# Kernel optimization log

Hardware: AMD Instinct MI355X
Metric: run time of the kernel (lower is better)

## Reference

```python
import jax, jax.numpy as jnp
import numpy as np

B, N, C = 8, 4096, 1024
H = 16
D = C // H  # head_dim = 64
SCALE = D ** -0.5


def setup_inputs() -> dict:
    key = jax.random.key(0)
    ks = jax.random.split(key, 5)
    s = 0.02
    return {
        "x": jax.random.normal(ks[0], (B, N, C), dtype=jnp.float32),
        "Wq": jax.random.normal(ks[1], (C, C), dtype=jnp.float32) * s,
        "Wk": jax.random.normal(ks[2], (C, C), dtype=jnp.float32) * s,
        "Wv": jax.random.normal(ks[3], (C, C), dtype=jnp.float32) * s,
        "Wp": jax.random.normal(ks[4], (C, C), dtype=jnp.float32) * s,
        "bp": jnp.zeros((C,), dtype=jnp.float32),
    }


def reference(x, Wq, Wk, Wv, Wp, bp):
    b, n, c = x.shape
    # nn.Linear: y = x @ W^T (no bias for q/k/v)
    def split_heads(y):
        # (B,N,C) -> (B,N,H,D) -> permute(0,2,3,1) -> (B,H,D,N)
        return jnp.transpose(y.reshape(b, n, H, D), (0, 2, 3, 1))

    q = split_heads(x @ Wq.T)  # (B,H,D,N)
    k = split_heads(x @ Wk.T)  # (B,H,D,N)
    v = split_heads(x @ Wv.T)  # (B,H,D,N)

    # attn over head_dim (faithful to source layout): (B,H,D,D)
    attn = jnp.einsum('bhdn,bhen->bhde', q, k) * SCALE
    attn = jax.nn.softmax(attn, axis=-1)
    # (B,H,D,D) @ (B,H,D,N) -> (B,H,D,N); transpose(1,2) -> (B,D,H,N); reshape (B,N,C)
    out = jnp.einsum('bhde,bhen->bhdn', attn, v)
    out = jnp.transpose(out, (0, 2, 1, 3)).reshape(b, n, c)
    return out @ Wp.T + bp
```

## Files before the change

kernel.cpp:

```cpp
#include <hip/hip_runtime.h>


typedef __attribute__((ext_vector_type(4))) float f32x4;
typedef __attribute__((ext_vector_type(8))) _Float16 f16x8;
typedef __attribute__((ext_vector_type(4))) unsigned short u16x4;
typedef __attribute__((ext_vector_type(8))) unsigned short u16x8;

__device__ __forceinline__ unsigned short f2h(float f) {
  union { _Float16 h; unsigned short u; } v;
  v.h = (_Float16)f;
  return v.u;
}

__global__ void cvt_f32_f16(const float* __restrict__ in, unsigned short* __restrict__ out, int n) {
  int i = (blockIdx.x * blockDim.x + threadIdx.x) * 4;
  if (i >= n) return;
  float4 v = *(const float4*)(in + i);
  u16x4 o;
  o.x = f2h(v.x); o.y = f2h(v.y); o.z = f2h(v.z); o.w = f2h(v.w);
  *(u16x4*)(out + i) = o;
}

__global__ void cvt4_f32_f16(const float* __restrict__ s0, const float* __restrict__ s1,
                             const float* __restrict__ s2, const float* __restrict__ s3,
                             unsigned short* __restrict__ d0, unsigned short* __restrict__ d1,
                             unsigned short* __restrict__ d2, unsigned short* __restrict__ d3) {
  const float* src; unsigned short* dst;
  switch (blockIdx.y) {
    case 0: src = s0; dst = d0; break;
    case 1: src = s1; dst = d1; break;
    case 2: src = s2; dst = d2; break;
    default: src = s3; dst = d3; break;
  }
  int i = (blockIdx.x * blockDim.x + threadIdx.x) * 4;
  float4 v = *(const float4*)(src + i);
  u16x4 o;
  o.x = f2h(v.x); o.y = f2h(v.y); o.z = f2h(v.z); o.w = f2h(v.w);
  *(u16x4*)(dst + i) = o;
}

enum { EPI_QKV = 0, EPI_F32_BIAS = 2 };

#define GLD(SRC, DST)                                                                   \
  __builtin_amdgcn_global_load_lds((const __attribute__((address_space(1))) void*)(SRC), \
                                   (__attribute__((address_space(3))) void*)(DST), 16, 0, 0)
#define SBAR() asm volatile("s_barrier" ::: "memory")

template <int EPI>
__global__ __launch_bounds__(512, 2) void gemm256(const unsigned short* __restrict__ A,
                                                  const unsigned short* __restrict__ Bt,
                                                  void* __restrict__ Cv,
                                                  const float* __restrict__ bias,
                                                  const int M, const int N, const int K) {
  __shared__ unsigned short lds[EPI == EPI_QKV ? 73728 : 65536];
  const int tid = threadIdx.x;
  const int w = tid >> 6, lane = tid & 63;
  const int quad = lane >> 4, l15 = lane & 15;
  const int wm = w >> 2, wn = w & 3;

  const int nt_n = N >> 8;
  const int cpx = (int)gridDim.x >> 3;
  const int xcd = (int)blockIdx.x & 7;
  const int lx = (int)blockIdx.x >> 3;
  const int strip = cpx / nt_n;
  const int per_bng = strip * 4;
  const int bng = lx / per_bng;
  const int r1 = lx - bng * per_bng;
  const int bmg = r1 >> 5;
  const int r2 = r1 & 31;
  const int bm = xcd * strip + bmg * 8 + (r2 & 7);
  const int bn = bng * 4 + (r2 >> 3);
  const int m0 = bm << 8, n0 = bn << 8;

  const int srow = lane >> 3;
  const unsigned short* aSrc = A + (size_t)(m0 + srow) * K + (((lane & 7) ^ srow) << 3);
  const unsigned short* bSrc = Bt + (size_t)(n0 + srow) * K + (((lane & 7) ^ srow) << 3);

  const int rbA = (w >> 2) * 128 + (w & 3) * 16;
  const int rbB = (w >> 1) * 64 + (w & 1) * 16;

  const int arow = (wm * 128 + l15) << 6;
  const int brow = (wn * 64 + l15) << 6;
  const int ak0 = (quad ^ (l15 & 7)) << 3;
  const int ak1 = ((4 + quad) ^ (l15 & 7)) << 3;

  f32x4 acc[8][4];
#pragma unroll
  for (int i = 0; i < 8; ++i)
#pragma unroll
    for (int j = 0; j < 4; ++j) acc[i][j] = f32x4{0.f, 0.f, 0.f, 0.f};
  f16x8 af[4][2], bf[2][2][2];

  const int NT = K >> 6;

  GLD(aSrc + (size_t)rbA * K, &lds[rbA * 64]);
  GLD(aSrc + (size_t)(rbA + 8) * K, &lds[(rbA + 8) * 64]);
  GLD(bSrc + (size_t)rbB * K, &lds[16384 + rbB * 64]);
  GLD(bSrc + (size_t)(rbB + 8) * K, &lds[16384 + (rbB + 8) * 64]);
  GLD(bSrc + (size_t)(rbB + 32) * K, &lds[16384 + (rbB + 32) * 64]);
  GLD(bSrc + (size_t)(rbB + 40) * K, &lds[16384 + (rbB + 40) * 64]);
  GLD(aSrc + (size_t)(rbA + 64) * K, &lds[(rbA + 64) * 64]);
  GLD(aSrc + (size_t)(rbA + 72) * K, &lds[(rbA + 72) * 64]);
  asm volatile("s_waitcnt vmcnt(4)" ::: "memory");
  SBAR();

  for (int t = 0; t < NT; ++t) {
    const int db = (t & 1) << 15;
    const int sb = ((t + 1) & 1) << 15;
    const int ks = (t + 1) << 6;
    const bool st = (t + 1) < NT;

#pragma unroll
    for (int mi = 0; mi < 4; ++mi) {
      af[mi][0] = *(const f16x8*)&lds[db + arow + mi * 1024 + ak0];
      af[mi][1] = *(const f16x8*)&lds[db + arow + mi * 1024 + ak1];
    }
#pragma unroll
    for (int nn = 0; nn < 2; ++nn) {
      bf[0][nn][0] = *(const f16x8*)&lds[db + 16384 + brow + nn * 1024 + ak0];
      bf[0][nn][1] = *(const f16x8*)&lds[db + 16384 + brow + nn * 1024 + ak1];
    }
    if (st) {
      GLD(aSrc + (size_t)rbA * K + ks, &lds[sb + rbA * 64]);
      GLD(aSrc + (size_t)(rbA + 8) * K + ks, &lds[sb + (rbA + 8) * 64]);
      GLD(bSrc + (size_t)rbB * K + ks, &lds[sb + 16384 + rbB * 64]);
      GLD(bSrc + (size_t)(rbB + 8) * K + ks, &lds[sb + 16384 + (rbB + 8) * 64]);
      GLD(bSrc + (size_t)(rbB + 32) * K + ks, &lds[sb + 16384 + (rbB + 32) * 64]);
      GLD(bSrc + (size_t)(rbB + 40) * K + ks, &lds[sb + 16384 + (rbB + 40) * 64]);
      GLD(aSrc + (size_t)(rbA + 64) * K + ks, &lds[sb + (rbA + 64) * 64]);
      GLD(aSrc + (size_t)(rbA + 72) * K + ks, &lds[sb + (rbA + 72) * 64]);
    }
    SBAR();
    __builtin_amdgcn_s_setprio(1);
#pragma unroll
    for (int s = 0; s < 2; ++s)
#pragma unroll
      for (int mi = 0; mi < 4; ++mi)
#pragma unroll
        for (int nn = 0; nn < 2; ++nn)
          acc[mi][nn] = __builtin_amdgcn_mfma_f32_16x16x32_f16(af[mi][s], bf[0][nn][s], acc[mi][nn], 0, 0, 0);
    __builtin_amdgcn_s_setprio(0);
    if (st) asm volatile("s_waitcnt vmcnt(10)" ::: "memory");
    else    asm volatile("s_waitcnt vmcnt(2)" ::: "memory");
    SBAR();

#pragma unroll
    for (int nn = 0; nn < 2; ++nn) {
      bf[1][nn][0] = *(const f16x8*)&lds[db + 16384 + brow + 2048 + nn * 1024 + ak0];
      bf[1][nn][1] = *(const f16x8*)&lds[db + 16384 + brow + 2048 + nn * 1024 + ak1];
    }
    SBAR();
    __builtin_amdgcn_s_setprio(1);
#pragma unroll
    for (int s = 0; s < 2; ++s)
#pragma unroll
      for (int mi = 0; mi < 4; ++mi)
#pragma unroll
        for (int nn = 0; nn < 2; ++nn)
          acc[mi][2 + nn] = __builtin_amdgcn_mfma_f32_16x16x32_f16(af[mi][s], bf[1][nn][s], acc[mi][2 + nn], 0, 0, 0);
    __builtin_amdgcn_s_setprio(0);
    if (st) asm volatile("s_waitcnt vmcnt(8)" ::: "memory");
    else    asm volatile("s_waitcnt vmcnt(0)" ::: "memory");
    SBAR();

#pragma unroll
    for (int mi = 0; mi < 4; ++mi) {
      af[mi][0] = *(const f16x8*)&lds[db + arow + 4096 + mi * 1024 + ak0];
      af[mi][1] = *(const f16x8*)&lds[db + arow + 4096 + mi * 1024 + ak1];
    }
    SBAR();
    __builtin_amdgcn_s_setprio(1);
#pragma unroll
    for (int s = 0; s < 2; ++s)
#pragma unroll
      for (int mi = 0; mi < 4; ++mi)
#pragma unroll
        for (int nn = 0; nn < 2; ++nn)
          acc[4 + mi][nn] = __builtin_amdgcn_mfma_f32_16x16x32_f16(af[mi][s], bf[0][nn][s], acc[4 + mi][nn], 0, 0, 0);
#pragma unroll
    for (int s = 0; s < 2; ++s)
#pragma unroll
      for (int mi = 0; mi < 4; ++mi)
#pragma unroll
        for (int nn = 0; nn < 2; ++nn)
          acc[4 + mi][2 + nn] = __builtin_amdgcn_mfma_f32_16x16x32_f16(af[mi][s], bf[1][nn][s], acc[4 + mi][2 + nn], 0, 0, 0);
    __builtin_amdgcn_s_setprio(0);
    if (st) asm volatile("s_waitcnt vmcnt(4)" ::: "memory");
    SBAR();
  }

  if (EPI == EPI_F32_BIAS) {
    float* C = (float*)Cv;
#pragma unroll
    for (int ni = 0; ni < 4; ++ni) {
      const int col = n0 + wn * 64 + ni * 16 + l15;
      const float bv = bias[col];
#pragma unroll
      for (int mi = 0; mi < 8; ++mi)
#pragma unroll
        for (int rr = 0; rr < 4; ++rr) {
          const int row = m0 + wm * 128 + mi * 16 + quad * 4 + rr;
          C[(size_t)row * N + col] = acc[mi][ni][rr] + bv;
        }
    }
  } else {
    unsigned short* C = (unsigned short*)Cv;
    const bool isT = (n0 < 2048);
    unsigned short* wreg = &lds[w * 9216];
    if (isT) {
#pragma unroll
      for (int mi = 0; mi < 8; ++mi)
#pragma unroll
        for (int ni = 0; ni < 4; ++ni) {
          u16x4 pk;
          pk.x = f2h(acc[mi][ni][0]); pk.y = f2h(acc[mi][ni][1]);
          pk.z = f2h(acc[mi][ni][2]); pk.w = f2h(acc[mi][ni][3]);
          *(u16x4*)&wreg[(ni * 16 + l15) * 136 + mi * 16 + quad * 4] = pk;
        }
#pragma unroll
      for (int p = 0; p < 16; ++p) {
        const int ch = p * 4 + quad;
        u16x8 v = *(const u16x8*)&wreg[ch * 136 + l15 * 8];
        *(u16x8*)&C[(size_t)(n0 + wn * 64 + ch) * M + m0 + wm * 128 + l15 * 8] = v;
      }
    } else {
#pragma unroll
      for (int mi = 0; mi < 8; ++mi)
#pragma unroll
        for (int ni = 0; ni < 4; ++ni)
#pragma unroll
          for (int rr = 0; rr < 4; ++rr)
            wreg[(mi * 16 + quad * 4 + rr) * 72 + ni * 16 + l15] = f2h(acc[mi][ni][rr]);
#pragma unroll
      for (int p = 0; p < 16; ++p) {
        const int tok = p * 8 + (lane >> 3);
        u16x8 v = *(const u16x8*)&wreg[tok * 72 + (lane & 7) * 8];
        *(u16x8*)&C[(size_t)2048 * M + (size_t)(m0 + wm * 128 + tok) * 1024 +
                    (n0 - 2048) + wn * 64 + (lane & 7) * 8] = v;
      }
    }
  }
}

__global__ __launch_bounds__(256) void attn_logits(const unsigned short* __restrict__ qkt,
                                                   float* __restrict__ pbuf) {
  const int h = blockIdx.x, b = blockIdx.y, s = blockIdx.z;
  const int tid = threadIdx.x;
  const int wave = tid >> 6, lane = tid & 63;
  const int quad = lane >> 4, l15 = lane & 15;

  f32x4 acc[4];
#pragma unroll
  for (int t = 0; t < 4; t++) acc[t] = f32x4{0.f, 0.f, 0.f, 0.f};

  const unsigned short* qp =
      qkt + (size_t)(h * 64 + wave * 16 + l15) * 32768 + b * 4096 + s * 256 + quad * 8;
  const unsigned short* kp[4];
#pragma unroll
  for (int et = 0; et < 4; et++)
    kp[et] = qkt + (size_t)(1024 + h * 64 + et * 16 + l15) * 32768 + b * 4096 + s * 256 + quad * 8;

#pragma unroll 2
  for (int k0 = 0; k0 < 256; k0 += 32) {
    f16x8 aq = *(const f16x8*)(qp + k0);
#pragma unroll
    for (int et = 0; et < 4; et++) {
      f16x8 bk = *(const f16x8*)(kp[et] + k0);
      acc[et] = __builtin_amdgcn_mfma_f32_16x16x32_f16(aq, bk, acc[et], 0, 0, 0);
    }
  }

  float* pb = pbuf + ((size_t)(b * 16 + h) * 16 + s) * 4096;
#pragma unroll
  for (int et = 0; et < 4; et++)
#pragma unroll
    for (int rr = 0; rr < 4; rr++)
      pb[(wave * 16 + quad * 4 + rr) * 64 + et * 16 + l15] = acc[et][rr];
}

__global__ __launch_bounds__(256) void attn_softmax(const float* __restrict__ pbuf,
                                                    unsigned short* __restrict__ pP) {
  const int bh = blockIdx.x >> 2, dg = blockIdx.x & 3;
  const int t = threadIdx.x;
  const int d = dg * 16 + (t >> 4), e4 = t & 15;
  const float* pb = pbuf + (size_t)bh * 65536 + d * 64 + e4 * 4;

  float v[4] = {0.f, 0.f, 0.f, 0.f};
  for (int s = 0; s < 16; s++) {
    float4 tt = *(const float4*)(pb + s * 4096);
    v[0] += tt.x; v[1] += tt.y; v[2] += tt.z; v[3] += tt.w;
  }
#pragma unroll
  for (int i = 0; i < 4; i++) v[i] *= 0.125f;

  float m = fmaxf(fmaxf(v[0], v[1]), fmaxf(v[2], v[3]));
#pragma unroll
  for (int o = 1; o < 16; o <<= 1) m = fmaxf(m, __shfl_xor(m, o, 16));
  float sum = 0.f;
#pragma unroll
  for (int i = 0; i < 4; i++) {
    v[i] = __expf(v[i] - m);
    sum += v[i];
  }
#pragma unroll
  for (int o = 1; o < 16; o <<= 1) sum += __shfl_xor(sum, o, 16);
  const float inv = 1.f / sum;

  u16x4 o4;
  o4.x = f2h(v[0] * inv); o4.y = f2h(v[1] * inv);
  o4.z = f2h(v[2] * inv); o4.w = f2h(v[3] * inv);
  *(u16x4*)(pP + (size_t)bh * 4096 + d * 64 + e4 * 4) = o4;
}

__global__ __launch_bounds__(256) void attn_pv(const unsigned short* __restrict__ pP,
                                               const unsigned short* __restrict__ vbuf,
                                               unsigned short* __restrict__ y) {
  __shared__ unsigned short tile[64 * 264];
  const int h = blockIdx.x, b = blockIdx.y, s = blockIdx.z;
  const int tid = threadIdx.x;
  const int wave = tid >> 6, lane = tid & 63;
  const int quad = lane >> 4, l15 = lane & 15;
  const int bh = b * 16 + h;

  const unsigned short* pp = pP + (size_t)bh * 4096 + (wave * 16 + l15) * 64 + quad * 8;
  f16x8 pa0 = *(const f16x8*)(pp);
  f16x8 pa1 = *(const f16x8*)(pp + 32);

  const unsigned short* vb =
      vbuf + (size_t)(b * 4096 + s * 256 + l15) * 1024 + h * 64 + quad * 8;

#pragma unroll 4
  for (int nt = 0; nt < 16; nt++) {
    const unsigned short* vp = vb + (size_t)nt * 16 * 1024;
    f16x8 v0 = *(const f16x8*)(vp);
    f16x8 v1 = *(const f16x8*)(vp + 32);
    f32x4 o = f32x4{0.f, 0.f, 0.f, 0.f};
    o = __builtin_amdgcn_mfma_f32_16x16x32_f16(pa0, v0, o, 0, 0, 0);
    o = __builtin_amdgcn_mfma_f32_16x16x32_f16(pa1, v1, o, 0, 0, 0);
    const int ncol = nt * 16 + l15;
#pragma unroll
    for (int rr = 0; rr < 4; rr++)
      tile[(wave * 16 + quad * 4 + rr) * 264 + ncol] = f2h(o[rr]);
  }
  __syncthreads();

  const int d = tid & 63, cc = tid >> 6;
  const int R = d * 64 + h * 4 + (s >> 2);
  unsigned short* dst =
      y + (size_t)b * 4194304 + (size_t)R * 1024 + (s & 3) * 256 + cc * 64;
  const unsigned short* srcp = &tile[d * 264 + cc * 64];
#pragma unroll
  for (int i = 0; i < 8; i++)
    *(u16x8*)(dst + i * 8) = *(const u16x8*)(srcp + i * 8);
}

extern "C" void kernel_launch(void* const* d_in, const int* in_sizes, int n_in, void* d_out,
                              int out_size, void* d_ws, size_t ws_size, hipStream_t stream) {
  (void)in_sizes; (void)n_in; (void)out_size; (void)ws_size;
  const float* x = (const float*)d_in[0];
  const float* Wq = (const float*)d_in[1];
  const float* Wk = (const float*)d_in[2];
  const float* Wv = (const float*)d_in[3];
  const float* Wp = (const float*)d_in[4];
  const float* bp = (const float*)d_in[5];

  char* ws = (char*)d_ws;
  unsigned short* xb = (unsigned short*)(ws);
  float* pbuf = (float*)(ws);
  unsigned short* yb = xb;
  unsigned short* qkt = (unsigned short*)(ws + (size_t)67108864);
  unsigned short* pP = qkt;
  unsigned short* vbuf = (unsigned short*)(ws + (size_t)201326592);
  unsigned short* wqkv = (unsigned short*)(ws + (size_t)268435456);
  unsigned short* wp = (unsigned short*)(ws + (size_t)274726912);

  cvt_f32_f16<<<32768, 256, 0, stream>>>(x, xb, 33554432);
  cvt4_f32_f16<<<dim3(1024, 4), 256, 0, stream>>>(Wq, Wk, Wv, Wp, wqkv, wqkv + 1048576,
                                                  wqkv + 2097152, wp);

  gemm256<EPI_QKV><<<1536, 512, 0, stream>>>(xb, wqkv, qkt, nullptr, 32768, 3072, 1024);

  attn_logits<<<dim3(16, 8, 16), 256, 0, stream>>>(qkt, pbuf);
  attn_softmax<<<512, 256, 0, stream>>>(pbuf, pP);
  attn_pv<<<dim3(16, 8, 16), 256, 0, stream>>>(pP, vbuf, yb);

  gemm256<EPI_F32_BIAS><<<512, 512, 0, stream>>>(yb, wp, (float*)d_out, bp, 32768, 1024, 1024);
}
```

Measured before the change: 645.8 us.

## Restructure GEMM main loop to prefetch next tile fragments and cut barriers

Reorganizes the double-buffered GEMM K-loop to hold separate register fragments for the low and high A halves and the two B halves. The first fragments of the next tile are loaded from LDS before the last MFMA block of the current iteration. The per-iteration barriers drop from five to two, and the global loads are split around the first MFMA block. The aim is to remove LDS-read stalls and barrier overhead between MFMA groups. In exchange it uses more fragment registers, which may lower occupancy. It also waits for all global loads (vmcnt(0)) at the end of each iteration, which may expose memory latency.

```diff
diff --git a/kernel.cpp b/kernel.cpp
--- a/kernel.cpp
+++ b/kernel.cpp
@@ -89,7 +89,7 @@
   for (int i = 0; i < 8; ++i)
 #pragma unroll
     for (int j = 0; j < 4; ++j) acc[i][j] = f32x4{0.f, 0.f, 0.f, 0.f};
-  f16x8 af[4][2], bf[2][2][2];
+  f16x8 al[4][2], ah[4][2], b0[2][2], b1[2][2];
 
   const int NT = K >> 6;
 
@@ -101,8 +101,18 @@
   GLD(bSrc + (size_t)(rbB + 40) * K, &lds[16384 + (rbB + 40) * 64]);
   GLD(aSrc + (size_t)(rbA + 64) * K, &lds[(rbA + 64) * 64]);
   GLD(aSrc + (size_t)(rbA + 72) * K, &lds[(rbA + 72) * 64]);
-  asm volatile("s_waitcnt vmcnt(4)" ::: "memory");
+  asm volatile("s_waitcnt vmcnt(0)" ::: "memory");
   SBAR();
+#pragma unroll
+  for (int mi = 0; mi < 4; ++mi) {
+    al[mi][0] = *(const f16x8*)&lds[arow + mi * 1024 + ak0];
+    al[mi][1] = *(const f16x8*)&lds[arow + mi * 1024 + ak1];
+  }
+#pragma unroll
+  for (int nn = 0; nn < 2; ++nn) {
+    b0[nn][0] = *(const f16x8*)&lds[16384 + brow + nn * 1024 + ak0];
+    b0[nn][1] = *(const f16x8*)&lds[16384 + brow + nn * 1024 + ak1];
+  }
 
   for (int t = 0; t < NT; ++t) {
     const int db = (t & 1) << 15;
@@ -111,26 +121,38 @@
     const bool st = (t + 1) < NT;
 
 #pragma unroll
+    for (int nn = 0; nn < 2; ++nn) {
+      b1[nn][0] = *(const f16x8*)&lds[db + 16384 + brow + 2048 + nn * 1024 + ak0];
+      b1[nn][1] = *(const f16x8*)&lds[db + 16384 + brow + 2048 + nn * 1024 + ak1];
+    }
+#pragma unroll
     for (int mi = 0; mi < 4; ++mi) {
-      af[mi][0] = *(const f16x8*)&lds[db + arow + mi * 1024 + ak0];
-      af[mi][1] = *(const f16x8*)&lds[db + arow + mi * 1024 + ak1];
-    }
-#pragma unroll
-    for (int nn = 0; nn < 2; ++nn) {
-      bf[0][nn][0] = *(const f16x8*)&lds[db + 16384 + brow + nn * 1024 + ak0];
-      bf[0][nn][1] = *(const f16x8*)&lds[db + 16384 + brow + nn * 1024 + ak1];
+      ah[mi][0] = *(const f16x8*)&lds[db + arow + 4096 + mi * 1024 + ak0];
+      ah[mi][1] = *(const f16x8*)&lds[db + arow + 4096 + mi * 1024 + ak1];
     }
     if (st) {
       GLD(aSrc + (size_t)rbA * K + ks, &lds[sb + rbA * 64]);
       GLD(aSrc + (size_t)(rbA + 8) * K + ks, &lds[sb + (rbA + 8) * 64]);
       GLD(bSrc + (size_t)rbB * K + ks, &lds[sb + 16384 + rbB * 64]);
       GLD(bSrc + (size_t)(rbB + 8) * K + ks, &lds[sb + 16384 + (rbB + 8) * 64]);
+    }
+
+    __builtin_amdgcn_s_setprio(1);
+#pragma unroll
+    for (int s = 0; s < 2; ++s)
+#pragma unroll
+      for (int mi = 0; mi < 4; ++mi)
+#pragma unroll
+        for (int nn = 0; nn < 2; ++nn)
+          acc[mi][nn] = __builtin_amdgcn_mfma_f32_16x16x32_f16(al[mi][s], b0[nn][s], acc[mi][nn], 0, 0, 0);
+    __builtin_amdgcn_s_setprio(0);
+    if (st) {
       GLD(bSrc + (size_t)(rbB + 32) * K + ks, &lds[sb + 16384 + (rbB + 32) * 64]);
       GLD(bSrc + (size_t)(rbB + 40) * K + ks, &lds[sb + 16384 + (rbB + 40) * 64]);
       GLD(aSrc + (size_t)(rbA + 64) * K + ks, &lds[sb + (rbA + 64) * 64]);
       GLD(aSrc + (size_t)(rbA + 72) * K + ks, &lds[sb + (rbA + 72) * 64]);
     }
-    SBAR();
+
     __builtin_amdgcn_s_setprio(1);
 #pragma unroll
     for (int s = 0; s < 2; ++s)
@@ -138,18 +160,9 @@
       for (int mi = 0; mi < 4; ++mi)
 #pragma unroll
         for (int nn = 0; nn < 2; ++nn)
-          acc[mi][nn] = __builtin_amdgcn_mfma_f32_16x16x32_f16(af[mi][s], bf[0][nn][s], acc[mi][nn], 0, 0, 0);
+          acc[mi][2 + nn] = __builtin_amdgcn_mfma_f32_16x16x32_f16(al[mi][s], b1[nn][s], acc[mi][2 + nn], 0, 0, 0);
     __builtin_amdgcn_s_setprio(0);
-    if (st) asm volatile("s_waitcnt vmcnt(10)" ::: "memory");
-    else    asm volatile("s_waitcnt vmcnt(2)" ::: "memory");
-    SBAR();
-
-#pragma unroll
-    for (int nn = 0; nn < 2; ++nn) {
-      bf[1][nn][0] = *(const f16x8*)&lds[db + 16384 + brow + 2048 + nn * 1024 + ak0];
-      bf[1][nn][1] = *(const f16x8*)&lds[db + 16384 + brow + 2048 + nn * 1024 + ak1];
-    }
-    SBAR();
+
     __builtin_amdgcn_s_setprio(1);
 #pragma unroll
     for (int s = 0; s < 2; ++s)
@@ -157,18 +170,26 @@
       for (int mi = 0; mi < 4; ++mi)
 #pragma unroll
         for (int nn = 0; nn < 2; ++nn)
-          acc[mi][2 + nn] = __builtin_amdgcn_mfma_f32_16x16x32_f16(af[mi][s], bf[1][nn][s], acc[mi][2 + nn], 0, 0, 0);
+          acc[4 + mi][nn] = __builtin_amdgcn_mfma_f32_16x16x32_f16(ah[mi][s], b0[nn][s], acc[4 + mi][nn], 0, 0, 0);
     __builtin_amdgcn_s_setprio(0);
-    if (st) asm volatile("s_waitcnt vmcnt(8)" ::: "memory");
+
+    if (st) asm volatile("s_waitcnt vmcnt(4)" ::: "memory");
     else    asm volatile("s_waitcnt vmcnt(0)" ::: "memory");
     SBAR();
 
-#pragma unroll
-    for (int mi = 0; mi < 4; ++mi) {
-      af[mi][0] = *(const f16x8*)&lds[db + arow + 4096 + mi * 1024 + ak0];
-      af[mi][1] = *(const f16x8*)&lds[db + arow + 4096 + mi * 1024 + ak1];
-    }
-    SBAR();
+    if (st) {
+#pragma unroll
+      for (int mi = 0; mi < 4; ++mi) {
+        al[mi][0] = *(const f16x8*)&lds[sb + arow + mi * 1024 + ak0];
+        al[mi][1] = *(const f16x8*)&lds[sb + arow + mi * 1024 + ak1];
+      }
+#pragma unroll
+      for (int nn = 0; nn < 2; ++nn) {
+        b0[nn][0] = *(const f16x8*)&lds[sb + 16384 + brow + nn * 1024 + ak0];
+        b0[nn][1] = *(const f16x8*)&lds[sb + 16384 + brow + nn * 1024 + ak1];
+      }
+    }
+
     __builtin_amdgcn_s_setprio(1);
 #pragma unroll
     for (int s = 0; s < 2; ++s)
@@ -176,16 +197,10 @@
       for (int mi = 0; mi < 4; ++mi)
 #pragma unroll
         for (int nn = 0; nn < 2; ++nn)
-          acc[4 + mi][nn] = __builtin_amdgcn_mfma_f32_16x16x32_f16(af[mi][s], bf[0][nn][s], acc[4 + mi][nn], 0, 0, 0);
-#pragma unroll
-    for (int s = 0; s < 2; ++s)
-#pragma unroll
-      for (int mi = 0; mi < 4; ++mi)
-#pragma unroll
-        for (int nn = 0; nn < 2; ++nn)
-          acc[4 + mi][2 + nn] = __builtin_amdgcn_mfma_f32_16x16x32_f16(af[mi][s], bf[1][nn][s], acc[4 + mi][2 + nn], 0, 0, 0);
+          acc[4 + mi][2 + nn] = __builtin_amdgcn_mfma_f32_16x16x32_f16(ah[mi][s], b1[nn][s], acc[4 + mi][2 + nn], 0, 0, 0);
     __builtin_amdgcn_s_setprio(0);
-    if (st) asm volatile("s_waitcnt vmcnt(4)" ::: "memory");
+
+    asm volatile("s_waitcnt vmcnt(0)" ::: "memory");
     SBAR();
   }
 
```

New measurement: 682.0 us. 5.6% more time.
